# Performance work log

Measured on AMD Instinct MI355X. Metric: run time of the kernel, lower is better.

Reference implementation:

```python
import jax, jax.numpy as jnp
import numpy as np

TOP_K = 2
LB_WEIGHT = 0.01
Z_WEIGHT = 0.001


def setup_inputs() -> dict:
    key = jax.random.key(0)
    ks = jax.random.split(key, 5)
    B, S, D, F, E = 4, 2048, 1024, 2048, 8
    x = jax.random.normal(ks[0], (B, S, D), dtype=jnp.float32)
    Wr = jax.random.normal(ks[1], (D, E), dtype=jnp.float32) / np.sqrt(D).astype(np.float32)
    Wg = jax.random.normal(ks[2], (E, D, F), dtype=jnp.float32) / np.sqrt(D).astype(np.float32)
    Wu = jax.random.normal(ks[3], (E, D, F), dtype=jnp.float32) / np.sqrt(D).astype(np.float32)
    Wd = jax.random.normal(ks[4], (E, F, D), dtype=jnp.float32) / np.sqrt(F).astype(np.float32)
    return {"x": x, "Wr": Wr, "Wg": Wg, "Wu": Wu, "Wd": Wd}


def reference(x, Wr, Wg, Wu, Wd):
    B, S, D = x.shape
    E = Wr.shape[1]
    xf = x.reshape(-1, D)                       # [T, D]
    T = xf.shape[0]

    logits = xf @ Wr                            # [T, E]
    probs = jax.nn.softmax(logits, axis=-1)
    topv, topi = jax.lax.top_k(probs, TOP_K)    # [T, K]
    topv = topv / jnp.sum(topv, axis=-1, keepdims=True)

    # combine[t, e] = renormalized top-k prob if expert e selected for token t, else 0
    onehot = jax.nn.one_hot(topi, E, dtype=x.dtype)          # [T, K, E]
    combine = jnp.sum(onehot * topv[..., None], axis=1)      # [T, E]

    out = jnp.zeros_like(xf)
    for e in range(E):  # fixed small expert count; dense compute masked by combine weights
        h = jax.nn.silu(xf @ Wg[e]) * (xf @ Wu[e])           # [T, F] SwiGLU
        out = out + combine[:, e:e + 1] * (h @ Wd[e])

    # auxiliary losses
    counts = jnp.sum(onehot, axis=(0, 1))                    # [E] tokens routed per expert
    f_i = counts / (T * TOP_K)
    P_i = jnp.mean(probs, axis=0)
    load_balance = E * jnp.sum(f_i * P_i)
    z_loss = jnp.mean(jax.nn.logsumexp(logits, axis=-1) ** 2)
    aux_loss = LB_WEIGHT * load_balance + Z_WEIGHT * z_loss

    return out.reshape(B, S, D), aux_loss
```

## Files before the change

### kernel.cpp

```cpp
#include <hip/hip_runtime.h>
#include <cstdint>

#define T_TOK 8192
#define Dm 1024
#define Fm 2048
#define Em 8

typedef unsigned short u16;
typedef __attribute__((ext_vector_type(8))) short short8;
typedef __attribute__((ext_vector_type(4))) float floatx4;

__device__ __forceinline__ u16 f2bf(float f) {
  union { float f; unsigned u; } v; v.f = f;
  unsigned r = v.u + 0x7fffu + ((v.u >> 16) & 1u);
  return (u16)(r >> 16);
}

__device__ __forceinline__ void gld_lds16(const void* g, void* l) {
  __builtin_amdgcn_global_load_lds(
      (const __attribute__((address_space(1))) void*)g,
      (__attribute__((address_space(3))) void*)l, 16, 0, 0);
}

__global__ void zero_meta(int* counts, int* offc, float* psum, float* zsum) {
  int t = threadIdx.x;
  if (t < 8) { counts[t] = 0; offc[t] = 0; psum[t] = 0.f; }
  if (t == 8) zsum[0] = 0.f;
}

__global__ __launch_bounds__(256) void convert_x_kernel(const float* __restrict__ x,
                                                        u16* __restrict__ xb) {
  int i = blockIdx.x * 256 + threadIdx.x;
  float4 v = ((const float4*)x)[i];
  unsigned lo = (unsigned)f2bf(v.x) | ((unsigned)f2bf(v.y) << 16);
  unsigned hi = (unsigned)f2bf(v.z) | ((unsigned)f2bf(v.w) << 16);
  ((uint2*)xb)[i] = make_uint2(lo, hi);
}

__global__ __launch_bounds__(256) void transpose_bf16(const float* __restrict__ src,
                                                      u16* __restrict__ dst, int R, int C) {
  __shared__ u16 tile[64 * 66];
  int e = blockIdx.z;
  int r0 = blockIdx.y * 64, c0 = blockIdx.x * 64;
  const float* s = src + (size_t)e * R * C;
  u16* d = dst + (size_t)e * C * R;
  int tid = threadIdx.x;
#pragma unroll
  for (int p = 0; p < 16; ++p) {
    int idx = p * 256 + tid;
    int i = idx >> 6, j = idx & 63;
    tile[i * 66 + j] = f2bf(s[(size_t)(r0 + i) * C + (c0 + j)]);
  }
  __syncthreads();
#pragma unroll
  for (int p = 0; p < 16; ++p) {
    int idx = p * 256 + tid;
    int i = idx >> 6, j = idx & 63;
    d[(size_t)(c0 + i) * R + (r0 + j)] = tile[j * 66 + i];
  }
}

__global__ __launch_bounds__(256) void router_kernel(
    const float* __restrict__ x, const float* __restrict__ Wr,
    int* __restrict__ topi, float* __restrict__ topw,
    int* __restrict__ counts, float* __restrict__ psum, float* __restrict__ zsum) {
  __shared__ float wr_s[Dm * Em];
  __shared__ float redf[4][9];
  __shared__ int redi[4][8];
  int tid = threadIdx.x;
  for (int i = tid; i < Dm * Em; i += 256) wr_s[i] = Wr[i];
  __syncthreads();
  int wv = tid >> 6, lane = tid & 63;
  float pl[8] = {0, 0, 0, 0, 0, 0, 0, 0};
  float zl = 0.f;
  int cl[8] = {0, 0, 0, 0, 0, 0, 0, 0};
  for (int it = 0; it < 8; ++it) {
    int t = (blockIdx.x * 4 + wv) * 8 + it;
    const float* xt = x + (size_t)t * Dm;
    float acc[8] = {0, 0, 0, 0, 0, 0, 0, 0};
#pragma unroll
    for (int i = 0; i < 16; ++i) {
      int dd = i * 64 + lane;
      float xv = xt[dd];
#pragma unroll
      for (int e2 = 0; e2 < 8; ++e2) acc[e2] += xv * wr_s[dd * 8 + e2];
    }
#pragma unroll
    for (int e2 = 0; e2 < 8; ++e2) {
      float v = acc[e2];
      for (int o = 32; o > 0; o >>= 1) v += __shfl_down(v, o);
      acc[e2] = v;
    }
    if (lane == 0) {
      float m = acc[0];
#pragma unroll
      for (int e2 = 1; e2 < 8; ++e2) m = fmaxf(m, acc[e2]);
      float p[8]; float s = 0.f;
#pragma unroll
      for (int e2 = 0; e2 < 8; ++e2) { p[e2] = expf(acc[e2] - m); s += p[e2]; }
      float inv = 1.f / s;
#pragma unroll
      for (int e2 = 0; e2 < 8; ++e2) { p[e2] *= inv; pl[e2] += p[e2]; }
      float lse = m + logf(s);
      zl += lse * lse;
      int i1 = 0;
#pragma unroll
      for (int e2 = 1; e2 < 8; ++e2) if (p[e2] > p[i1]) i1 = e2;
      int i2 = -1; float b2 = -1e30f;
#pragma unroll
      for (int e2 = 0; e2 < 8; ++e2)
        if (e2 != i1 && p[e2] > b2) { b2 = p[e2]; i2 = e2; }
      float ssum = p[i1] + p[i2];
      topi[2 * t] = i1; topi[2 * t + 1] = i2;
      topw[2 * t] = p[i1] / ssum; topw[2 * t + 1] = p[i2] / ssum;
      cl[i1]++; cl[i2]++;
    }
  }
  if (lane == 0) {
#pragma unroll
    for (int e2 = 0; e2 < 8; ++e2) { redf[wv][e2] = pl[e2]; redi[wv][e2] = cl[e2]; }
    redf[wv][8] = zl;
  }
  __syncthreads();
  if (tid < 8) {
    atomicAdd(&psum[tid], redf[0][tid] + redf[1][tid] + redf[2][tid] + redf[3][tid]);
    atomicAdd(&counts[tid], redi[0][tid] + redi[1][tid] + redi[2][tid] + redi[3][tid]);
  } else if (tid == 8) {
    atomicAdd(zsum, redf[0][8] + redf[1][8] + redf[2][8] + redf[3][8]);
  }
}

__global__ void finalize_kernel(const int* counts, const float* psum, const float* zsum,
                                int* bases, float* out_aux) {
  if (threadIdx.x == 0) {
    int b = 0;
    for (int e = 0; e < 8; ++e) { bases[e] = b; b += counts[e]; }
    bases[8] = b;
    float lb = 0.f;
    for (int e = 0; e < 8; ++e)
      lb += ((float)counts[e] / (2.f * T_TOK)) * (psum[e] / (float)T_TOK);
    lb *= 8.f;
    float z = zsum[0] / (float)T_TOK;
    *out_aux = 0.01f * lb + 0.001f * z;
  }
}

__global__ __launch_bounds__(256) void scatter_kernel(
    const int* __restrict__ topi, const float* __restrict__ topw,
    const int* __restrict__ bases, int* __restrict__ offc,
    int* __restrict__ etok, float* __restrict__ ew) {
  __shared__ int lcnt[8];
  __shared__ int lbase[8];
  int tid = threadIdx.x;
  if (tid < 8) lcnt[tid] = 0;
  __syncthreads();
  int t = blockIdx.x * 256 + tid;
  int e0 = topi[2 * t], e1 = topi[2 * t + 1];
  int lp0 = atomicAdd(&lcnt[e0], 1);
  int lp1 = atomicAdd(&lcnt[e1], 1);
  __syncthreads();
  if (tid < 8) lbase[tid] = atomicAdd(&offc[tid], lcnt[tid]);
  __syncthreads();
  int p0 = bases[e0] + lbase[e0] + lp0;
  etok[p0] = t; ew[p0] = topw[2 * t];
  int p1 = bases[e1] + lbase[e1] + lp1;
  etok[p1] = t; ew[p1] = topw[2 * t + 1];
}

__global__ __launch_bounds__(256, 2) void gemm1_kernel(
    const u16* __restrict__ xb, const u16* __restrict__ WgT, const u16* __restrict__ WuT,
    u16* __restrict__ h, const int* __restrict__ etok,
    const int* __restrict__ counts, const int* __restrict__ bases) {
  const int e = blockIdx.z;
  const int Ne = counts[e];
  const int m0 = blockIdx.y * 128;
  if (m0 >= Ne) return;
  const int n0 = blockIdx.x * 128;
  const int be = bases[e];

  __shared__ __align__(16) u16 As[128 * 64];
  __shared__ __align__(16) u16 Bgs[128 * 64];
  __shared__ __align__(16) u16 Bus[128 * 64];

  const int tid = threadIdx.x;
  const int wv = tid >> 6, lane = tid & 63;
  const int wr = wv >> 1, wc = wv & 1;

  const int srow = tid >> 3;
  const int cg = (tid & 7) ^ (srow & 7);
  const u16* wg_e = WgT + (size_t)e * Fm * Dm;
  const u16* wu_e = WuT + (size_t)e * Fm * Dm;

  const u16* ag[4]; const u16* bgp[4]; const u16* bup[4];
#pragma unroll
  for (int j = 0; j < 4; ++j) {
    int row = 32 * j + srow;
    int rr = m0 + row; rr = rr < Ne ? rr : Ne - 1;
    int tok = etok[be + rr];
    ag[j] = xb + (size_t)tok * Dm + cg * 8;
    bgp[j] = wg_e + (size_t)(n0 + row) * Dm + cg * 8;
    bup[j] = wu_e + (size_t)(n0 + row) * Dm + cg * 8;
  }
  const int lbase = 8 * wv * 64 + lane * 8;

  floatx4 accg[4][4], accu[4][4];
#pragma unroll
  for (int mi = 0; mi < 4; ++mi)
#pragma unroll
    for (int ni = 0; ni < 4; ++ni) { accg[mi][ni] = (floatx4)0.f; accu[mi][ni] = (floatx4)0.f; }

  for (int k0 = 0; k0 < Dm; k0 += 64) {
    __syncthreads();
#pragma unroll
    for (int j = 0; j < 4; ++j) {
      int lo = lbase + 32 * j * 64;
      gld_lds16(ag[j] + k0, &As[lo]);
      gld_lds16(bgp[j] + k0, &Bgs[lo]);
      gld_lds16(bup[j] + k0, &Bus[lo]);
    }
    __syncthreads();
#pragma unroll
    for (int ks = 0; ks < 2; ++ks) {
      short8 af[4], bgf[4], buf_[4];
      const int col = lane & 15, quad = lane >> 4;
      const int c = ks * 4 + quad;
#pragma unroll
      for (int mi = 0; mi < 4; ++mi) {
        int row = wr * 64 + mi * 16 + col;
        af[mi] = *(const short8*)&As[row * 64 + ((c ^ (row & 7)) << 3)];
      }
#pragma unroll
      for (int ni = 0; ni < 4; ++ni) {
        int row = wc * 64 + ni * 16 + col;
        int o = row * 64 + ((c ^ (row & 7)) << 3);
        bgf[ni] = *(const short8*)&Bgs[o];
        buf_[ni] = *(const short8*)&Bus[o];
      }
#pragma unroll
      for (int mi = 0; mi < 4; ++mi)
#pragma unroll
        for (int ni = 0; ni < 4; ++ni) {
          accg[mi][ni] = __builtin_amdgcn_mfma_f32_16x16x32_bf16(af[mi], bgf[ni], accg[mi][ni], 0, 0, 0);
          accu[mi][ni] = __builtin_amdgcn_mfma_f32_16x16x32_bf16(af[mi], buf_[ni], accu[mi][ni], 0, 0, 0);
        }
    }
  }
  const int col = lane & 15, quad = lane >> 4;
#pragma unroll
  for (int mi = 0; mi < 4; ++mi)
#pragma unroll
    for (int ni = 0; ni < 4; ++ni) {
      int f = n0 + wc * 64 + ni * 16 + col;
#pragma unroll
      for (int r = 0; r < 4; ++r) {
        int lrow = wr * 64 + mi * 16 + quad * 4 + r;
        if (m0 + lrow < Ne) {
          float gv = accg[mi][ni][r];
          float hv = (gv / (1.f + expf(-gv))) * accu[mi][ni][r];
          h[(size_t)(be + m0 + lrow) * Fm + f] = f2bf(hv);
        }
      }
    }
}

__global__ __launch_bounds__(256, 2) void gemm2_kernel(
    const u16* __restrict__ h, const u16* __restrict__ WdT, float* __restrict__ out,
    const int* __restrict__ etok, const float* __restrict__ ew,
    const int* __restrict__ counts, const int* __restrict__ bases) {
  const int e = blockIdx.z;
  const int Ne = counts[e];
  const int m0 = blockIdx.y * 128;
  if (m0 >= Ne) return;
  const int n0 = blockIdx.x * 128;
  const int be = bases[e];

  __shared__ __align__(16) u16 As[128 * 64];
  __shared__ __align__(16) u16 Bs[128 * 64];
  __shared__ int tokS[128];
  __shared__ float wS[128];

  const int tid = threadIdx.x;
  if (tid < 128) {
    int rr = m0 + tid; rr = rr < Ne ? rr : Ne - 1;
    tokS[tid] = etok[be + rr];
    wS[tid] = ew[be + rr];
  }
  const int wv = tid >> 6, lane = tid & 63;
  const int wr = wv >> 1, wc = wv & 1;
  const int srow = tid >> 3;
  const int cg = (tid & 7) ^ (srow & 7);
  const u16* wd_e = WdT + (size_t)e * Dm * Fm;

  const u16* ap[4]; const u16* bp[4];
#pragma unroll
  for (int j = 0; j < 4; ++j) {
    int row = 32 * j + srow;
    int rr = m0 + row; rr = rr < Ne ? rr : Ne - 1;
    ap[j] = h + (size_t)(be + rr) * Fm + cg * 8;
    bp[j] = wd_e + (size_t)(n0 + row) * Fm + cg * 8;
  }
  const int lbase = 8 * wv * 64 + lane * 8;

  floatx4 acc[4][4];
#pragma unroll
  for (int mi = 0; mi < 4; ++mi)
#pragma unroll
    for (int ni = 0; ni < 4; ++ni) acc[mi][ni] = (floatx4)0.f;

  for (int k0 = 0; k0 < Fm; k0 += 64) {
    __syncthreads();
#pragma unroll
    for (int j = 0; j < 4; ++j) {
      int lo = lbase + 32 * j * 64;
      gld_lds16(ap[j] + k0, &As[lo]);
      gld_lds16(bp[j] + k0, &Bs[lo]);
    }
    __syncthreads();
#pragma unroll
    for (int ks = 0; ks < 2; ++ks) {
      short8 af[4], bf[4];
      const int col = lane & 15, quad = lane >> 4;
      const int c = ks * 4 + quad;
#pragma unroll
      for (int mi = 0; mi < 4; ++mi) {
        int row = wr * 64 + mi * 16 + col;
        af[mi] = *(const short8*)&As[row * 64 + ((c ^ (row & 7)) << 3)];
      }
#pragma unroll
      for (int ni = 0; ni < 4; ++ni) {
        int row = wc * 64 + ni * 16 + col;
        bf[ni] = *(const short8*)&Bs[row * 64 + ((c ^ (row & 7)) << 3)];
      }
#pragma unroll
      for (int mi = 0; mi < 4; ++mi)
#pragma unroll
        for (int ni = 0; ni < 4; ++ni)
          acc[mi][ni] = __builtin_amdgcn_mfma_f32_16x16x32_bf16(af[mi], bf[ni], acc[mi][ni], 0, 0, 0);
    }
  }
  const int col = lane & 15, quad = lane >> 4;
#pragma unroll
  for (int mi = 0; mi < 4; ++mi)
#pragma unroll
    for (int ni = 0; ni < 4; ++ni) {
      int oc = n0 + wc * 64 + ni * 16 + col;
#pragma unroll
      for (int r = 0; r < 4; ++r) {
        int lrow = wr * 64 + mi * 16 + quad * 4 + r;
        if (m0 + lrow < Ne) {
          float v = acc[mi][ni][r] * wS[lrow];
          atomicAdd(&out[(size_t)tokS[lrow] * Dm + oc], v);
        }
      }
    }
}

extern "C" void kernel_launch(void* const* d_in, const int* in_sizes, int n_in,
                              void* d_out, int out_size, void* d_ws, size_t ws_size,
                              hipStream_t stream) {
  const float* x = (const float*)d_in[0];
  const float* Wr = (const float*)d_in[1];
  const float* Wg = (const float*)d_in[2];
  const float* Wu = (const float*)d_in[3];
  const float* Wd = (const float*)d_in[4];
  float* out = (float*)d_out;

  char* p = (char*)d_ws;
  auto take = [&](size_t bytes) { char* r = p; p += (bytes + 255) & ~(size_t)255; return r; };
  u16* xb = (u16*)take((size_t)T_TOK * Dm * 2);
  u16* WgT = (u16*)take((size_t)Em * Fm * Dm * 2);
  u16* WuT = (u16*)take((size_t)Em * Fm * Dm * 2);
  u16* WdT = (u16*)take((size_t)Em * Dm * Fm * 2);
  u16* h = (u16*)take((size_t)2 * T_TOK * Fm * 2);
  int* topi = (int*)take((size_t)T_TOK * 2 * 4);
  float* topw = (float*)take((size_t)T_TOK * 2 * 4);
  int* etok = (int*)take((size_t)2 * T_TOK * 4);
  float* ew = (float*)take((size_t)2 * T_TOK * 4);
  int* counts = (int*)take(64);
  int* bases = (int*)take(64);
  int* offc = (int*)take(64);
  float* psum = (float*)take(64);
  float* zsum = (float*)take(64);

  hipMemsetAsync(d_out, 0, (size_t)out_size * 4, stream);
  zero_meta<<<1, 64, 0, stream>>>(counts, offc, psum, zsum);
  convert_x_kernel<<<dim3((T_TOK * Dm / 4) / 256), 256, 0, stream>>>(x, xb);
  transpose_bf16<<<dim3(Fm / 64, Dm / 64, Em), 256, 0, stream>>>(Wg, WgT, Dm, Fm);
  transpose_bf16<<<dim3(Fm / 64, Dm / 64, Em), 256, 0, stream>>>(Wu, WuT, Dm, Fm);
  transpose_bf16<<<dim3(Dm / 64, Fm / 64, Em), 256, 0, stream>>>(Wd, WdT, Fm, Dm);
  router_kernel<<<dim3(T_TOK / 32), 256, 0, stream>>>(x, Wr, topi, topw, counts, psum, zsum);
  finalize_kernel<<<1, 64, 0, stream>>>(counts, psum, zsum, bases, out + (size_t)T_TOK * Dm);
  scatter_kernel<<<dim3(T_TOK / 256), 256, 0, stream>>>(topi, topw, bases, offc, etok, ew);
  gemm1_kernel<<<dim3(Fm / 128, 64, Em), 256, 0, stream>>>(xb, WgT, WuT, h, etok, counts, bases);
  gemm2_kernel<<<dim3(Dm / 128, 64, Em), 256, 0, stream>>>(h, WdT, out, etok, ew, counts, bases);
}
```

Baseline: 593.8 us.

## Fuse x conversion into router, merge weight transposes, raise GEMM occupancy bounds

The three weight transpose launches become a single transpose_all kernel that picks its matrix and tile from a flat block index. The standalone x-to-bf16 conversion kernel is removed; the router now writes the bf16 copy of x while it already reads x for the logits. The launch-bounds occupancy hints are raised on gemm1 (to 3) and gemm2 (to 4), which cuts launch overhead and one full read of x but may force register spills in the GEMMs.

```diff
diff --git a/kernel.cpp b/kernel.cpp
--- a/kernel.cpp
+++ b/kernel.cpp
@@ -28,20 +28,20 @@
   if (t == 8) zsum[0] = 0.f;
 }
 
-__global__ __launch_bounds__(256) void convert_x_kernel(const float* __restrict__ x,
-                                                        u16* __restrict__ xb) {
-  int i = blockIdx.x * 256 + threadIdx.x;
-  float4 v = ((const float4*)x)[i];
-  unsigned lo = (unsigned)f2bf(v.x) | ((unsigned)f2bf(v.y) << 16);
-  unsigned hi = (unsigned)f2bf(v.z) | ((unsigned)f2bf(v.w) << 16);
-  ((uint2*)xb)[i] = make_uint2(lo, hi);
-}
-
-__global__ __launch_bounds__(256) void transpose_bf16(const float* __restrict__ src,
-                                                      u16* __restrict__ dst, int R, int C) {
+__global__ __launch_bounds__(256) void transpose_all(
+    const float* __restrict__ Wg, const float* __restrict__ Wu, const float* __restrict__ Wd,
+    u16* __restrict__ WgT, u16* __restrict__ WuT, u16* __restrict__ WdT) {
   __shared__ u16 tile[64 * 66];
-  int e = blockIdx.z;
-  int r0 = blockIdx.y * 64, c0 = blockIdx.x * 64;
+  int bid = blockIdx.x;
+  int m = bid >> 9;
+  int t = bid & 511;
+  int type = m >> 3, e = m & 7;
+  const float* src; u16* dst; int R, C, csh;
+  if (type == 0)      { src = Wg; dst = WgT; R = Dm; C = Fm; csh = 5; }
+  else if (type == 1) { src = Wu; dst = WuT; R = Dm; C = Fm; csh = 5; }
+  else                { src = Wd; dst = WdT; R = Fm; C = Dm; csh = 4; }
+  int ty = t >> csh, tx = t & ((1 << csh) - 1);
+  int r0 = ty * 64, c0 = tx * 64;
   const float* s = src + (size_t)e * R * C;
   u16* d = dst + (size_t)e * C * R;
   int tid = threadIdx.x;
@@ -62,6 +62,7 @@
 
 __global__ __launch_bounds__(256) void router_kernel(
     const float* __restrict__ x, const float* __restrict__ Wr,
+    u16* __restrict__ xb,
     int* __restrict__ topi, float* __restrict__ topw,
     int* __restrict__ counts, float* __restrict__ psum, float* __restrict__ zsum) {
   __shared__ float wr_s[Dm * Em];
@@ -77,11 +78,13 @@
   for (int it = 0; it < 8; ++it) {
     int t = (blockIdx.x * 4 + wv) * 8 + it;
     const float* xt = x + (size_t)t * Dm;
+    u16* xbt = xb + (size_t)t * Dm;
     float acc[8] = {0, 0, 0, 0, 0, 0, 0, 0};
 #pragma unroll
     for (int i = 0; i < 16; ++i) {
       int dd = i * 64 + lane;
       float xv = xt[dd];
+      xbt[dd] = f2bf(xv);
 #pragma unroll
       for (int e2 = 0; e2 < 8; ++e2) acc[e2] += xv * wr_s[dd * 8 + e2];
     }
@@ -167,7 +170,7 @@
   etok[p1] = t; ew[p1] = topw[2 * t + 1];
 }
 
-__global__ __launch_bounds__(256, 2) void gemm1_kernel(
+__global__ __launch_bounds__(256, 3) void gemm1_kernel(
     const u16* __restrict__ xb, const u16* __restrict__ WgT, const u16* __restrict__ WuT,
     u16* __restrict__ h, const int* __restrict__ etok,
     const int* __restrict__ counts, const int* __restrict__ bases) {
@@ -263,7 +266,7 @@
     }
 }
 
-__global__ __launch_bounds__(256, 2) void gemm2_kernel(
+__global__ __launch_bounds__(256, 4) void gemm2_kernel(
     const u16* __restrict__ h, const u16* __restrict__ WdT, float* __restrict__ out,
     const int* __restrict__ etok, const float* __restrict__ ew,
     const int* __restrict__ counts, const int* __restrict__ bases) {
@@ -384,11 +387,8 @@
 
   hipMemsetAsync(d_out, 0, (size_t)out_size * 4, stream);
   zero_meta<<<1, 64, 0, stream>>>(counts, offc, psum, zsum);
-  convert_x_kernel<<<dim3((T_TOK * Dm / 4) / 256), 256, 0, stream>>>(x, xb);
-  transpose_bf16<<<dim3(Fm / 64, Dm / 64, Em), 256, 0, stream>>>(Wg, WgT, Dm, Fm);
-  transpose_bf16<<<dim3(Fm / 64, Dm / 64, Em), 256, 0, stream>>>(Wu, WuT, Dm, Fm);
-  transpose_bf16<<<dim3(Dm / 64, Fm / 64, Em), 256, 0, stream>>>(Wd, WdT, Fm, Dm);
-  router_kernel<<<dim3(T_TOK / 32), 256, 0, stream>>>(x, Wr, topi, topw, counts, psum, zsum);
+  transpose_all<<<dim3(24 * 512), 256, 0, stream>>>(Wg, Wu, Wd, WgT, WuT, WdT);
+  router_kernel<<<dim3(T_TOK / 32), 256, 0, stream>>>(x, Wr, xb, topi, topw, counts, psum, zsum);
   finalize_kernel<<<1, 64, 0, stream>>>(counts, psum, zsum, bases, out + (size_t)T_TOK * Dm);
   scatter_kernel<<<dim3(T_TOK / 256), 256, 0, stream>>>(topi, topw, bases, offc, etok, ew);
   gemm1_kernel<<<dim3(Fm / 128, 64, Em), 256, 0, stream>>>(xb, WgT, WuT, h, etok, counts, bases);
```

Result: slower. 1.077 ms (+81.4%).
